# Optimization experiments

Hardware: AMD Instinct MI355X
Metric: run time of the kernel (lower is better)

## Reference

```python
import jax, jax.numpy as jnp
import numpy as np

N_HEAD = 16

def setup_inputs() -> dict:
    key = jax.random.key(0)
    k1, k2, k3 = jax.random.split(key, 3)
    B, T, C = 2, 2048, 1024
    x = jax.random.normal(k1, (B, T, C), dtype=jnp.float32)
    W_attn = jax.random.normal(k2, (C, 3 * C), dtype=jnp.float32) * (C ** -0.5)
    b_attn = jnp.zeros((3 * C,), dtype=jnp.float32)
    W_proj = jax.random.normal(k3, (C, C), dtype=jnp.float32) * (C ** -0.5)
    b_proj = jnp.zeros((C,), dtype=jnp.float32)
    return {"x": x, "W_attn": W_attn, "b_attn": b_attn, "W_proj": W_proj, "b_proj": b_proj}

def reference(x, W_attn, b_attn, W_proj, b_proj):
    B, T, C = x.shape
    H = N_HEAD
    D = C // H  # head_dim
    scale = D ** -0.5
    qkv = x @ W_attn + b_attn                       # [B,T,3C]
    q, k, v = jnp.split(qkv, 3, axis=-1)
    # [B,T,C] -> [B,H,T,D]
    q = q.reshape(B, T, H, D).transpose(0, 2, 1, 3)
    k = k.reshape(B, T, H, D).transpose(0, 2, 1, 3)
    v = v.reshape(B, T, H, D).transpose(0, 2, 1, 3)
    att = jnp.einsum('bhqd,bhkd->bhqk', q, k) * scale
    causal = jnp.tril(jnp.ones((T, T), dtype=bool))
    att = jnp.where(causal, att, jnp.float32(-jnp.inf))
    att = jax.nn.softmax(att, axis=-1)
    y = jnp.einsum('bhqk,bhkd->bhqd', att, v)       # [B,H,T,D]
    y = y.transpose(0, 2, 1, 3).reshape(B, T, C)
    return y @ W_proj + b_proj
```

## Files before the change

### kernel.cpp

```cpp
#include <hip/hip_runtime.h>

typedef __bf16 bf16;
typedef __bf16 bf16x4 __attribute__((ext_vector_type(4)));
typedef __bf16 bf16x8 __attribute__((ext_vector_type(8)));
typedef short s16x4 __attribute__((ext_vector_type(4)));
typedef float f32x4 __attribute__((ext_vector_type(4)));
typedef unsigned int u32x4 __attribute__((ext_vector_type(4)));

#define NB 2
#define NT 2048
#define NC 1024
#define NH 16
#define ND 64

#if __has_builtin(__builtin_amdgcn_exp2f)
#define EXP2F(x) __builtin_amdgcn_exp2f(x)
#else
#define EXP2F(x) __expf(0.69314718055994531f * (x))
#endif

#if __has_builtin(__builtin_amdgcn_rcpf)
#define RCPF(x) __builtin_amdgcn_rcpf(x)
#else
#define RCPF(x) (1.0f / (x))
#endif

__device__ __forceinline__ void async16(const void* g, void* l) {
  __builtin_amdgcn_global_load_lds(
      (const __attribute__((address_space(1))) void*)g,
      (__attribute__((address_space(3))) void*)l, 16, 0, 0);
}

__device__ __forceinline__ bf16x8 ld8(const bf16* p) {
  return *reinterpret_cast<const bf16x8*>(p);
}
__device__ __forceinline__ bf16x4 ld4(const bf16* p) {
  return *reinterpret_cast<const bf16x4*>(p);
}

__device__ __forceinline__ f32x4 mfma16(bf16x4 a, bf16x4 b, f32x4 c) {
  s16x4 ai = __builtin_bit_cast(s16x4, a);
  s16x4 bi = __builtin_bit_cast(s16x4, b);
#if __has_builtin(__builtin_amdgcn_mfma_f32_16x16x16bf16_1k)
  return __builtin_amdgcn_mfma_f32_16x16x16bf16_1k(ai, bi, c, 0, 0, 0);
#else
  f32x4 d;
  asm("v_mfma_f32_16x16x16_bf16 %0, %1, %2, %3"
      : "=v"(d) : "v"(ai), "v"(bi), "v"(c));
  return d;
#endif
}

__global__ __launch_bounds__(256) void prep(
    const float* __restrict__ x, bf16* __restrict__ xb,
    const float* __restrict__ Wa, bf16* __restrict__ Da,
    const float* __restrict__ Wp, bf16* __restrict__ Dp) {
  int bx = blockIdx.x;
  if (bx < 2048) {
    int i = (bx * 256 + threadIdx.x) * 8;
    const float4* s = (const float4*)(x + i);
    float4 a = s[0], b = s[1];
    bf16x8 o;
    o[0] = (bf16)a.x; o[1] = (bf16)a.y; o[2] = (bf16)a.z; o[3] = (bf16)a.w;
    o[4] = (bf16)b.x; o[5] = (bf16)b.y; o[6] = (bf16)b.z; o[7] = (bf16)b.w;
    *(bf16x8*)(xb + i) = o;
    return;
  }
  __shared__ float tile[32][33];
  int idx = bx - 2048;
  const float* src;
  bf16* dst;
  int Cc, cb, rb;
  if (idx < 96 * 32) { src = Wa; dst = Da; Cc = 3072; cb = idx % 96; rb = idx / 96; }
  else { idx -= 96 * 32; src = Wp; dst = Dp; Cc = 1024; cb = idx % 32; rb = idx / 32; }
  int tx = threadIdx.x & 31, ty = threadIdx.x >> 5;
  int r0 = rb * 32, c0 = cb * 32;
#pragma unroll
  for (int i = 0; i < 4; ++i)
    tile[ty + i * 8][tx] = src[(size_t)(r0 + ty + i * 8) * Cc + c0 + tx];
  __syncthreads();
#pragma unroll
  for (int i = 0; i < 4; ++i)
    dst[(size_t)(c0 + ty + i * 8) * 1024 + r0 + tx] = (bf16)tile[tx][ty + i * 8];
}

__global__ __launch_bounds__(256, 3) void gemm_qkv(
    const bf16* __restrict__ A,
    const bf16* __restrict__ Bt,
    const float* __restrict__ bias,
    bf16* __restrict__ Qo, bf16* __restrict__ Ko, bf16* __restrict__ Vto) {
  const int K = 1024;
  __shared__ bf16 As[128 * 32];
  __shared__ bf16 Bs[128 * 32];
  const int tid = threadIdx.x;
  const int lane = tid & 63, wv = tid >> 6;
  const int quad = lane >> 4, ln = lane & 15;
  const int m0 = blockIdx.x * 128, n0 = blockIdx.y * 128;
  const int wr = (wv >> 1) * 64, wc = (wv & 1) * 64;
  const int rA = tid >> 2, cA = (tid & 3) * 8;
  f32x4 acc[4][4] = {};

  for (int kt = 0; kt < K / 32; ++kt) {
    const int k0 = kt * 32;
#pragma unroll
    for (int inst = 0; inst < 2; ++inst) {
      async16(A + (size_t)(m0 + inst * 64 + rA) * K + k0 + cA,
              &As[inst * 2048 + wv * 512]);
      async16(Bt + (size_t)(n0 + inst * 64 + rA) * K + k0 + cA,
              &Bs[inst * 2048 + wv * 512]);
    }
    __syncthreads();
    bf16x8 aF[4], bF[4];
#pragma unroll
    for (int i = 0; i < 4; ++i) {
      aF[i] = ld8(&As[(wr + i * 16 + ln) * 32 + quad * 8]);
      bF[i] = ld8(&Bs[(wc + i * 16 + ln) * 32 + quad * 8]);
    }
#pragma unroll
    for (int rb = 0; rb < 4; ++rb)
#pragma unroll
      for (int cb = 0; cb < 4; ++cb)
        acc[rb][cb] = __builtin_amdgcn_mfma_f32_16x16x32_bf16(
            aF[rb], bF[cb], acc[rb][cb], 0, 0, 0);
    __syncthreads();
  }
#pragma unroll
  for (int rb = 0; rb < 4; ++rb) {
#pragma unroll
    for (int cb = 0; cb < 4; ++cb) {
      int gn = n0 + wc + cb * 16 + ln;
      int part = gn >> 10, c = gn & 1023;
      int h = c >> 6, dd = c & 63;
      float bs = bias[gn];
      int gm0 = m0 + wr + rb * 16 + quad * 4;
      int b = gm0 >> 11, t0 = gm0 & 2047;
      if (part == 2) {
        bf16x4 vv;
#pragma unroll
        for (int r = 0; r < 4; ++r) vv[r] = (bf16)(acc[rb][cb][r] + bs);
        *(bf16x4*)(Vto + ((size_t)(b * NH + h) * ND + dd) * NT + t0) = vv;
      } else {
        bf16* dst = part == 0 ? Qo : Ko;
        float sc = part == 0 ? 0.18033688f : 1.0f;
#pragma unroll
        for (int r = 0; r < 4; ++r)
          dst[((size_t)(b * NH + h) * NT + t0 + r) * ND + dd] =
              (bf16)((acc[rb][cb][r] + bs) * sc);
      }
    }
  }
}

__global__ __launch_bounds__(256, 3) void flash_attn_kernel(
    const bf16* __restrict__ Qg, const bf16* __restrict__ Kg,
    const bf16* __restrict__ Vtg, bf16* __restrict__ Yg) {
  __shared__ __align__(16) char smem[2][16384];
  const int tid = threadIdx.x;
  const int lane = tid & 63, wv = tid >> 6;
  const int quad = lane >> 4, ln = lane & 15;
  const int bid = blockIdx.x;
  const int qt = 15 - (bid >> 5);
  const int bh = bid & 31;
  const int bb = bh >> 4, hh = bh & 15;
  const int q0w = qt * 128 + wv * 32;
  const bf16* Qp = Qg + ((size_t)bh * NT + q0w) * ND;
  const bf16* Kbase = Kg + (size_t)bh * NT * ND;
  const bf16* Vtbase = Vtg + (size_t)bh * ND * NT;

  const int sub = lane >> 3, sch = lane & 7;
  const int swz = ln & 7;

  bf16x8 qf[2][2];
#pragma unroll
  for (int qb = 0; qb < 2; ++qb)
#pragma unroll
    for (int ks = 0; ks < 2; ++ks)
      qf[qb][ks] = ld8(Qp + (size_t)(qb * 16 + ln) * ND + ks * 32 + quad * 8);

  f32x4 oacc[2][4] = {};
  float li[2] = {0.f, 0.f};

  const int ktiles = 2 * qt + 2;
  const int cw = 2 * qt + 1 + (wv >> 1);

#define STAGE(KT, P)                                                           \
  {                                                                            \
    const int k0s = (KT) * 64;                                                 \
    char* Kl = smem[P];                                                        \
    char* Vl = smem[P] + 8192;                                                 \
    int r0s = wv * 16 + sub;                                                   \
    int gch = sch ^ sub;                                                       \
    async16(Kbase + (size_t)(k0s + r0s) * ND + gch * 8, Kl + wv * 16 * 128);   \
    async16(Kbase + (size_t)(k0s + r0s + 8) * ND + gch * 8,                    \
            Kl + wv * 16 * 128 + 1024);                                        \
    async16(Vtbase + (size_t)r0s * NT + k0s + gch * 8, Vl + wv * 16 * 128);    \
    async16(Vtbase + (size_t)(r0s + 8) * NT + k0s + gch * 8,                   \
            Vl + wv * 16 * 128 + 1024);                                        \
  }

  STAGE(0, 0);
  for (int kt = 0; kt < ktiles; ++kt) {
    const int p = kt & 1;
    __syncthreads();
    if (kt + 1 < ktiles) STAGE(kt + 1, p ^ 1);
    if (kt < cw) {
      const char* Kl = smem[p];
      const char* Vl = smem[p] + 8192;
      const int k0 = kt * 64;
      f32x4 sacc[2][4] = {};
#pragma unroll
      for (int ks = 0; ks < 2; ++ks) {
        bf16x8 kfr[4];
#pragma unroll
        for (int cb = 0; cb < 4; ++cb)
          kfr[cb] = *(const bf16x8*)(Kl + (cb * 16 + ln) * 128 +
                                     (((ks * 4 + quad) ^ swz) * 16));
#pragma unroll
        for (int qb = 0; qb < 2; ++qb)
#pragma unroll
          for (int cb = 0; cb < 4; ++cb)
            sacc[qb][cb] = __builtin_amdgcn_mfma_f32_16x16x32_bf16(
                kfr[cb], qf[qb][ks], sacc[qb][cb], 0, 0, 0);
      }
      if (k0 + 63 > q0w) {
#pragma unroll
        for (int qb = 0; qb < 2; ++qb) {
          int qr = q0w + qb * 16 + ln;
#pragma unroll
          for (int cb = 0; cb < 4; ++cb)
#pragma unroll
            for (int r = 0; r < 4; ++r) {
              int kc = k0 + cb * 16 + quad * 4 + r;
              if (kc > qr) sacc[qb][cb][r] = -1e30f;
            }
        }
      }
      bf16x4 pf[2][4];
#pragma unroll
      for (int qb = 0; qb < 2; ++qb) {
        float rs = 0.f;
#pragma unroll
        for (int cb = 0; cb < 4; ++cb) {
          bf16x4 pv;
#pragma unroll
          for (int r = 0; r < 4; ++r) {
            float pexp = EXP2F(sacc[qb][cb][r]);
            rs += pexp;
            pv[r] = (bf16)pexp;
          }
          pf[qb][cb] = pv;
        }
        li[qb] += rs;
      }
#pragma unroll
      for (int cb = 0; cb < 4; ++cb) {
        bf16x4 vfr[4];
#pragma unroll
        for (int db = 0; db < 4; ++db)
          vfr[db] = *(const bf16x4*)(Vl + (db * 16 + ln) * 128 +
                                     (((cb * 2 + (quad >> 1)) ^ swz) * 16) +
                                     (quad & 1) * 8);
#pragma unroll
        for (int qb = 0; qb < 2; ++qb)
#pragma unroll
          for (int db = 0; db < 4; ++db)
            oacc[qb][db] = mfma16(vfr[db], pf[qb][cb], oacc[qb][db]);
      }
    }
  }
#undef STAGE

#pragma unroll
  for (int qb = 0; qb < 2; ++qb) {
    float l = li[qb];
    l += __shfl_xor(l, 16);
    l += __shfl_xor(l, 32);
    float inv = RCPF(l);
    int row = q0w + qb * 16 + ln;
#pragma unroll
    for (int db = 0; db < 4; ++db) {
      bf16x4 ov;
#pragma unroll
      for (int r = 0; r < 4; ++r) ov[r] = (bf16)(oacc[qb][db][r] * inv);
      *(bf16x4*)(Yg + ((size_t)(bb * NT + row)) * NC + hh * 64 + db * 16 +
                 quad * 4) = ov;
    }
  }
}

__global__ __launch_bounds__(256, 2) void gemm_proj(
    const bf16* __restrict__ A,
    const bf16* __restrict__ Bt,
    const float* __restrict__ bias,
    float* __restrict__ out) {
  const int K = 1024;
  __shared__ bf16 As[128 * 32];
  __shared__ bf16 Bs[64 * 32];
  const int tid = threadIdx.x;
  const int lane = tid & 63, wv = tid >> 6;
  const int quad = lane >> 4, ln = lane & 15;
  const int m0 = blockIdx.x * 128, n0 = blockIdx.y * 64;
  const int wr = wv * 32;
  const int rA = tid >> 2, cA = (tid & 3) * 8;
  f32x4 acc[2][4] = {};

  for (int kt = 0; kt < K / 32; ++kt) {
    const int k0 = kt * 32;
#pragma unroll
    for (int inst = 0; inst < 2; ++inst)
      async16(A + (size_t)(m0 + inst * 64 + rA) * K + k0 + cA,
              &As[inst * 2048 + wv * 512]);
    async16(Bt + (size_t)(n0 + rA) * K + k0 + cA, &Bs[wv * 512]);
    __syncthreads();
    bf16x8 aF[2], bF[4];
#pragma unroll
    for (int i = 0; i < 2; ++i)
      aF[i] = ld8(&As[(wr + i * 16 + ln) * 32 + quad * 8]);
#pragma unroll
    for (int i = 0; i < 4; ++i)
      bF[i] = ld8(&Bs[(i * 16 + ln) * 32 + quad * 8]);
#pragma unroll
    for (int rb = 0; rb < 2; ++rb)
#pragma unroll
      for (int cb = 0; cb < 4; ++cb)
        acc[rb][cb] = __builtin_amdgcn_mfma_f32_16x16x32_bf16(
            aF[rb], bF[cb], acc[rb][cb], 0, 0, 0);
    __syncthreads();
  }
#pragma unroll
  for (int rb = 0; rb < 2; ++rb) {
#pragma unroll
    for (int cb = 0; cb < 4; ++cb) {
      int gn = n0 + cb * 16 + ln;
      float bs = bias[gn];
#pragma unroll
      for (int r = 0; r < 4; ++r) {
        int gm = m0 + wr + rb * 16 + quad * 4 + r;
        out[(size_t)gm * 1024 + gn] = acc[rb][cb][r] + bs;
      }
    }
  }
}

extern "C" void kernel_launch(void* const* d_in, const int* in_sizes, int n_in,
                              void* d_out, int out_size, void* d_ws, size_t ws_size,
                              hipStream_t stream) {
  const float* x      = (const float*)d_in[0];
  const float* W_attn = (const float*)d_in[1];
  const float* b_attn = (const float*)d_in[2];
  const float* W_proj = (const float*)d_in[3];
  const float* b_proj = (const float*)d_in[4];
  float* out = (float*)d_out;

  bf16* ws  = (bf16*)d_ws;
  bf16* xb  = ws;
  bf16* Wab = xb + (size_t)4096 * 1024;
  bf16* Wpb = Wab + (size_t)3072 * 1024;
  bf16* Qb  = Wpb + (size_t)1024 * 1024;
  bf16* Kb  = Qb + (size_t)32 * 2048 * 64;
  bf16* Vtb = Kb + (size_t)32 * 2048 * 64;
  bf16* Yb  = xb;

  prep<<<2048 + 96 * 32 + 32 * 32, 256, 0, stream>>>(x, xb, W_attn, Wab,
                                                     W_proj, Wpb);
  gemm_qkv<<<dim3(32, 24), 256, 0, stream>>>(xb, Wab, b_attn, Qb, Kb, Vtb);
  flash_attn_kernel<<<512, 256, 0, stream>>>(Qb, Kb, Vtb, Yb);
  gemm_proj<<<dim3(32, 16), 256, 0, stream>>>(Yb, Wpb, b_proj, out);
}
```

Before: 167.8 us.

## Rework QKV GEMM into 256x256 double-buffered swizzled tiles with interleaved staging

The QKV projection GEMM moves from 128x128 tiles with 256 threads and single-buffered BK=32 LDS to 256x256 tiles with 512 threads and BK=64. LDS is double-buffered and XOR-swizzled to avoid bank conflicts, and the loads for the next k-tile are interleaved with four MFMA quadrants using s_setprio and partial vmcnt waits. The aim is more operand reuse per LDS load and hiding global-load latency behind MFMA work. In exchange, the grid shrinks to 192 blocks, fewer than the CU count, and the 128KB of LDS per block limits residency to one block per CU.

Result: slower. 178.1 us (+6.1%).

```diff
diff --git a/kernel.cpp b/kernel.cpp
--- a/kernel.cpp
+++ b/kernel.cpp
@@ -33,9 +33,6 @@
 
 __device__ __forceinline__ bf16x8 ld8(const bf16* p) {
   return *reinterpret_cast<const bf16x8*>(p);
-}
-__device__ __forceinline__ bf16x4 ld4(const bf16* p) {
-  return *reinterpret_cast<const bf16x4*>(p);
 }
 
 __device__ __forceinline__ f32x4 mfma16(bf16x4 a, bf16x4 b, f32x4 c) {
@@ -49,6 +46,13 @@
       : "=v"(d) : "v"(ai), "v"(bi), "v"(c));
   return d;
 #endif
+}
+
+__device__ __forceinline__ bf16x8 ldfrag(const bf16* buf, int row, int ks,
+                                         int quad) {
+  int byte = (row * 128 + ks * 64 + quad * 16) ^ ((row & 7) << 4);
+  return *reinterpret_cast<const bf16x8*>(
+      reinterpret_cast<const char*>(buf) + byte);
 }
 
 __global__ __launch_bounds__(256) void prep(
@@ -84,68 +88,139 @@
     dst[(size_t)(c0 + ty + i * 8) * 1024 + r0 + tx] = (bf16)tile[tx][ty + i * 8];
 }
 
-__global__ __launch_bounds__(256, 3) void gemm_qkv(
+__global__ __launch_bounds__(512, 2) void gemm_qkv(
     const bf16* __restrict__ A,
     const bf16* __restrict__ Bt,
     const float* __restrict__ bias,
     bf16* __restrict__ Qo, bf16* __restrict__ Ko, bf16* __restrict__ Vto) {
-  const int K = 1024;
-  __shared__ bf16 As[128 * 32];
-  __shared__ bf16 Bs[128 * 32];
+  __shared__ __align__(16) bf16 As_[2][256 * 64];
+  __shared__ __align__(16) bf16 Bs_[2][256 * 64];
   const int tid = threadIdx.x;
   const int lane = tid & 63, wv = tid >> 6;
+  const int wm = wv >> 2, wn = wv & 3;
   const int quad = lane >> 4, ln = lane & 15;
-  const int m0 = blockIdx.x * 128, n0 = blockIdx.y * 128;
-  const int wr = (wv >> 1) * 64, wc = (wv & 1) * 64;
-  const int rA = tid >> 2, cA = (tid & 3) * 8;
-  f32x4 acc[4][4] = {};
-
-  for (int kt = 0; kt < K / 32; ++kt) {
-    const int k0 = kt * 32;
-#pragma unroll
-    for (int inst = 0; inst < 2; ++inst) {
-      async16(A + (size_t)(m0 + inst * 64 + rA) * K + k0 + cA,
-              &As[inst * 2048 + wv * 512]);
-      async16(Bt + (size_t)(n0 + inst * 64 + rA) * K + k0 + cA,
-              &Bs[inst * 2048 + wv * 512]);
-    }
-    __syncthreads();
-    bf16x8 aF[4], bF[4];
-#pragma unroll
-    for (int i = 0; i < 4; ++i) {
-      aF[i] = ld8(&As[(wr + i * 16 + ln) * 32 + quad * 8]);
-      bF[i] = ld8(&Bs[(wc + i * 16 + ln) * 32 + quad * 8]);
-    }
-#pragma unroll
-    for (int rb = 0; rb < 4; ++rb)
-#pragma unroll
-      for (int cb = 0; cb < 4; ++cb)
-        acc[rb][cb] = __builtin_amdgcn_mfma_f32_16x16x32_bf16(
-            aF[rb], bF[cb], acc[rb][cb], 0, 0, 0);
-    __syncthreads();
-  }
-#pragma unroll
-  for (int rb = 0; rb < 4; ++rb) {
-#pragma unroll
-    for (int cb = 0; cb < 4; ++cb) {
-      int gn = n0 + wc + cb * 16 + ln;
-      int part = gn >> 10, c = gn & 1023;
-      int h = c >> 6, dd = c & 63;
-      float bs = bias[gn];
-      int gm0 = m0 + wr + rb * 16 + quad * 4;
-      int b = gm0 >> 11, t0 = gm0 & 2047;
-      if (part == 2) {
-        bf16x4 vv;
-#pragma unroll
-        for (int r = 0; r < 4; ++r) vv[r] = (bf16)(acc[rb][cb][r] + bs);
-        *(bf16x4*)(Vto + ((size_t)(b * NH + h) * ND + dd) * NT + t0) = vv;
-      } else {
-        bf16* dst = part == 0 ? Qo : Ko;
-        float sc = part == 0 ? 0.18033688f : 1.0f;
-#pragma unroll
-        for (int r = 0; r < 4; ++r)
-          dst[((size_t)(b * NH + h) * NT + t0 + r) * ND + dd] =
-              (bf16)((acc[rb][cb][r] + bs) * sc);
+  const int m0 = blockIdx.x * 256, n0 = blockIdx.y * 256;
+
+#define STAGE_A(tt, h, p)                                                     \
+  {                                                                           \
+    int rl = lane >> 3, ch = (lane & 7) ^ rl;                                 \
+    const bf16* g = A + (size_t)(m0 + (h) * 128 + wv * 8 + rl) * 1024 +       \
+                    (tt) * 64 + ch * 8;                                       \
+    bf16* lp = &As_[p][((h) * 128 + wv * 8) * 64];                            \
+    async16(g, lp);                                                           \
+    async16(g + (size_t)64 * 1024, lp + 64 * 64);                             \
+  }
+#define STAGE_B(tt, h, p)                                                     \
+  {                                                                           \
+    int rl = lane >> 3, ch = (lane & 7) ^ rl;                                 \
+    const bf16* g = Bt + (size_t)(n0 + (h) * 128 + wv * 8 + rl) * 1024 +      \
+                    (tt) * 64 + ch * 8;                                       \
+    bf16* lp = &Bs_[p][((h) * 128 + wv * 8) * 64];                            \
+    async16(g, lp);                                                           \
+    async16(g + (size_t)64 * 1024, lp + 64 * 64);                             \
+  }
+
+  f32x4 acc[2][2][4][2] = {};
+  bf16x8 aF[4][2], bF0[2][2], bF1[2][2];
+
+#define MFMA_Q(MH, NH, BF)                                                    \
+  __builtin_amdgcn_s_setprio(1);                                              \
+  _Pragma("unroll") for (int ks = 0; ks < 2; ++ks)                            \
+      _Pragma("unroll") for (int mm = 0; mm < 4; ++mm)                        \
+          _Pragma("unroll") for (int nn = 0; nn < 2; ++nn)                    \
+              acc[MH][NH][mm][nn] = __builtin_amdgcn_mfma_f32_16x16x32_bf16(  \
+                  aF[mm][ks], BF[nn][ks], acc[MH][NH][mm][nn], 0, 0, 0);      \
+  __builtin_amdgcn_s_setprio(0);
+
+  STAGE_A(0, 0, 0);
+  STAGE_B(0, 0, 0);
+  STAGE_B(0, 1, 0);
+  STAGE_A(0, 1, 0);
+  asm volatile("s_waitcnt vmcnt(4)" ::: "memory");
+  __builtin_amdgcn_s_barrier();
+
+  for (int t = 0; t < 16; ++t) {
+    const bf16* Ap = As_[t & 1];
+    const bf16* Bp = Bs_[t & 1];
+    const int pn = (t & 1) ^ 1;
+    const bool more = (t + 1) < 16;
+
+#pragma unroll
+    for (int mm = 0; mm < 4; ++mm)
+#pragma unroll
+      for (int ks = 0; ks < 2; ++ks)
+        aF[mm][ks] = ldfrag(Ap, wm * 64 + mm * 16 + ln, ks, quad);
+#pragma unroll
+    for (int nn = 0; nn < 2; ++nn)
+#pragma unroll
+      for (int ks = 0; ks < 2; ++ks)
+        bF0[nn][ks] = ldfrag(Bp, wn * 32 + nn * 16 + ln, ks, quad);
+    if (more) STAGE_A(t + 1, 0, pn);
+    __builtin_amdgcn_s_barrier();
+    MFMA_Q(0, 0, bF0);
+    asm volatile("s_waitcnt vmcnt(4)" ::: "memory");
+    __builtin_amdgcn_s_barrier();
+
+#pragma unroll
+    for (int nn = 0; nn < 2; ++nn)
+#pragma unroll
+      for (int ks = 0; ks < 2; ++ks)
+        bF1[nn][ks] = ldfrag(Bp, 128 + wn * 32 + nn * 16 + ln, ks, quad);
+    if (more) STAGE_B(t + 1, 0, pn);
+    __builtin_amdgcn_s_barrier();
+    MFMA_Q(0, 1, bF1);
+    asm volatile("s_waitcnt vmcnt(4)" ::: "memory");
+    __builtin_amdgcn_s_barrier();
+
+#pragma unroll
+    for (int mm = 0; mm < 4; ++mm)
+#pragma unroll
+      for (int ks = 0; ks < 2; ++ks)
+        aF[mm][ks] = ldfrag(Ap, 128 + wm * 64 + mm * 16 + ln, ks, quad);
+    if (more) STAGE_B(t + 1, 1, pn);
+    __builtin_amdgcn_s_barrier();
+    MFMA_Q(1, 1, bF1);
+    __builtin_amdgcn_s_barrier();
+
+    if (more) STAGE_A(t + 1, 1, pn);
+    __builtin_amdgcn_s_barrier();
+    MFMA_Q(1, 0, bF0);
+    asm volatile("s_waitcnt vmcnt(4)" ::: "memory");
+    __builtin_amdgcn_s_barrier();
+  }
+#undef STAGE_A
+#undef STAGE_B
+#undef MFMA_Q
+
+#pragma unroll
+  for (int MH = 0; MH < 2; ++MH) {
+#pragma unroll
+    for (int NHh = 0; NHh < 2; ++NHh) {
+#pragma unroll
+      for (int mm = 0; mm < 4; ++mm) {
+#pragma unroll
+        for (int nn = 0; nn < 2; ++nn) {
+          int gn = n0 + NHh * 128 + wn * 32 + nn * 16 + ln;
+          int part = gn >> 10, c = gn & 1023;
+          int h = c >> 6, dd = c & 63;
+          float bs = bias[gn];
+          int gm0 = m0 + MH * 128 + wm * 64 + mm * 16 + quad * 4;
+          int b = gm0 >> 11, t0 = gm0 & 2047;
+          if (part == 2) {
+            bf16x4 vv;
+#pragma unroll
+            for (int r = 0; r < 4; ++r)
+              vv[r] = (bf16)(acc[MH][NHh][mm][nn][r] + bs);
+            *(bf16x4*)(Vto + ((size_t)(b * NH + h) * ND + dd) * NT + t0) = vv;
+          } else {
+            bf16* dst = part == 0 ? Qo : Ko;
+            float sc = part == 0 ? 0.18033688f : 1.0f;
+#pragma unroll
+            for (int r = 0; r < 4; ++r)
+              dst[((size_t)(b * NH + h) * NT + t0 + r) * ND + dd] =
+                  (bf16)((acc[MH][NHh][mm][nn][r] + bs) * sc);
+          }
+        }
       }
     }
   }
@@ -363,7 +438,7 @@
 
   prep<<<2048 + 96 * 32 + 32 * 32, 256, 0, stream>>>(x, xb, W_attn, Wab,
                                                      W_proj, Wpb);
-  gemm_qkv<<<dim3(32, 24), 256, 0, stream>>>(xb, Wab, b_attn, Qb, Kb, Vtb);
+  gemm_qkv<<<dim3(16, 12), 512, 0, stream>>>(xb, Wab, b_attn, Qb, Kb, Vtb);
   flash_attn_kernel<<<512, 256, 0, stream>>>(Qb, Kb, Vtb, Yb);
   gemm_proj<<<dim3(32, 16), 256, 0, stream>>>(Yb, Wpb, b_proj, out);
 }
```

## Pair low and high causal query tiles per block to balance attention work

Applied to the files above, without the earlier changes.

Each flash-attention block now handles two 16-row query slices per wave, one from a low query tile and one from the mirrored high tile, split into two halves. The goal is to give every block a similar amount of causal work and remove the load imbalance from blocks ordered by query tile. Each block still streams K/V up to the high tile, and the low slice switches off once it is past its causal limit. This adds divergent-free but branchy MFMA issue, and the low slice does no useful work for much of the loop.

After: 357.7 us. +113.2%, slower.

```diff
diff --git a/kernel.cpp b/kernel.cpp
--- a/kernel.cpp
+++ b/kernel.cpp
@@ -33,9 +33,6 @@
 
 __device__ __forceinline__ bf16x8 ld8(const bf16* p) {
   return *reinterpret_cast<const bf16x8*>(p);
-}
-__device__ __forceinline__ bf16x4 ld4(const bf16* p) {
-  return *reinterpret_cast<const bf16x4*>(p);
 }
 
 __device__ __forceinline__ f32x4 mfma16(bf16x4 a, bf16x4 b, f32x4 c) {
@@ -159,11 +156,15 @@
   const int lane = tid & 63, wv = tid >> 6;
   const int quad = lane >> 4, ln = lane & 15;
   const int bid = blockIdx.x;
-  const int qt = 15 - (bid >> 5);
   const int bh = bid & 31;
+  const int pr = (bid >> 5) & 7;
+  const int half = bid >> 8;
   const int bb = bh >> 4, hh = bh & 15;
-  const int q0w = qt * 128 + wv * 32;
-  const bf16* Qp = Qg + ((size_t)bh * NT + q0w) * ND;
+  const int qLo = pr, qHi = 15 - pr;
+  const int q0l = qLo * 128 + half * 64 + wv * 16;
+  const int q0h = qHi * 128 + half * 64 + wv * 16;
+  const bf16* QpL = Qg + ((size_t)bh * NT + q0l) * ND;
+  const bf16* QpH = Qg + ((size_t)bh * NT + q0h) * ND;
   const bf16* Kbase = Kg + (size_t)bh * NT * ND;
   const bf16* Vtbase = Vtg + (size_t)bh * ND * NT;
 
@@ -172,16 +173,17 @@
 
   bf16x8 qf[2][2];
 #pragma unroll
-  for (int qb = 0; qb < 2; ++qb)
-#pragma unroll
-    for (int ks = 0; ks < 2; ++ks)
-      qf[qb][ks] = ld8(Qp + (size_t)(qb * 16 + ln) * ND + ks * 32 + quad * 8);
+  for (int ks = 0; ks < 2; ++ks) {
+    qf[0][ks] = ld8(QpL + (size_t)ln * ND + ks * 32 + quad * 8);
+    qf[1][ks] = ld8(QpH + (size_t)ln * ND + ks * 32 + quad * 8);
+  }
 
   f32x4 oacc[2][4] = {};
   float li[2] = {0.f, 0.f};
 
-  const int ktiles = 2 * qt + 2;
-  const int cw = 2 * qt + 1 + (wv >> 1);
+  const int ktiles = 2 * qHi + 2;
+  const int cw0 = 2 * qLo + half + 1;
+  const int cw1 = 2 * qHi + half + 1;
 
 #define STAGE(KT, P)                                                           \
   {                                                                            \
@@ -203,7 +205,8 @@
     const int p = kt & 1;
     __syncthreads();
     if (kt + 1 < ktiles) STAGE(kt + 1, p ^ 1);
-    if (kt < cw) {
+    if (kt < cw1) {
+      const bool act0 = kt < cw0;
       const char* Kl = smem[p];
       const char* Vl = smem[p] + 8192;
       const int k0 = kt * 64;
@@ -216,41 +219,64 @@
           kfr[cb] = *(const bf16x8*)(Kl + (cb * 16 + ln) * 128 +
                                      (((ks * 4 + quad) ^ swz) * 16));
 #pragma unroll
-        for (int qb = 0; qb < 2; ++qb)
-#pragma unroll
-          for (int cb = 0; cb < 4; ++cb)
-            sacc[qb][cb] = __builtin_amdgcn_mfma_f32_16x16x32_bf16(
-                kfr[cb], qf[qb][ks], sacc[qb][cb], 0, 0, 0);
-      }
-      if (k0 + 63 > q0w) {
-#pragma unroll
-        for (int qb = 0; qb < 2; ++qb) {
-          int qr = q0w + qb * 16 + ln;
-#pragma unroll
-          for (int cb = 0; cb < 4; ++cb)
-#pragma unroll
-            for (int r = 0; r < 4; ++r) {
-              int kc = k0 + cb * 16 + quad * 4 + r;
-              if (kc > qr) sacc[qb][cb][r] = -1e30f;
-            }
+        for (int cb = 0; cb < 4; ++cb) {
+          sacc[1][cb] = __builtin_amdgcn_mfma_f32_16x16x32_bf16(
+              kfr[cb], qf[1][ks], sacc[1][cb], 0, 0, 0);
+          if (act0)
+            sacc[0][cb] = __builtin_amdgcn_mfma_f32_16x16x32_bf16(
+                kfr[cb], qf[0][ks], sacc[0][cb], 0, 0, 0);
         }
       }
+      if (k0 + 63 > q0h) {
+        int qr = q0h + ln;
+#pragma unroll
+        for (int cb = 0; cb < 4; ++cb)
+#pragma unroll
+          for (int r = 0; r < 4; ++r) {
+            int kc = k0 + cb * 16 + quad * 4 + r;
+            if (kc > qr) sacc[1][cb][r] = -1e30f;
+          }
+      }
+      if (act0 && k0 + 63 > q0l) {
+        int qr = q0l + ln;
+#pragma unroll
+        for (int cb = 0; cb < 4; ++cb)
+#pragma unroll
+          for (int r = 0; r < 4; ++r) {
+            int kc = k0 + cb * 16 + quad * 4 + r;
+            if (kc > qr) sacc[0][cb][r] = -1e30f;
+          }
+      }
       bf16x4 pf[2][4];
-#pragma unroll
-      for (int qb = 0; qb < 2; ++qb) {
+      {
         float rs = 0.f;
 #pragma unroll
         for (int cb = 0; cb < 4; ++cb) {
           bf16x4 pv;
 #pragma unroll
           for (int r = 0; r < 4; ++r) {
-            float pexp = EXP2F(sacc[qb][cb][r]);
+            float pexp = EXP2F(sacc[1][cb][r]);
             rs += pexp;
             pv[r] = (bf16)pexp;
           }
-          pf[qb][cb] = pv;
+          pf[1][cb] = pv;
         }
-        li[qb] += rs;
+        li[1] += rs;
+      }
+      if (act0) {
+        float rs = 0.f;
+#pragma unroll
+        for (int cb = 0; cb < 4; ++cb) {
+          bf16x4 pv;
+#pragma unroll
+          for (int r = 0; r < 4; ++r) {
+            float pexp = EXP2F(sacc[0][cb][r]);
+            rs += pexp;
+            pv[r] = (bf16)pexp;
+          }
+          pf[0][cb] = pv;
+        }
+        li[0] += rs;
       }
 #pragma unroll
       for (int cb = 0; cb < 4; ++cb) {
@@ -261,10 +287,12 @@
                                      (((cb * 2 + (quad >> 1)) ^ swz) * 16) +
                                      (quad & 1) * 8);
 #pragma unroll
-        for (int qb = 0; qb < 2; ++qb)
+        for (int db = 0; db < 4; ++db)
+          oacc[1][db] = mfma16(vfr[db], pf[1][cb], oacc[1][db]);
+        if (act0)
 #pragma unroll
           for (int db = 0; db < 4; ++db)
-            oacc[qb][db] = mfma16(vfr[db], pf[qb][cb], oacc[qb][db]);
+            oacc[0][db] = mfma16(vfr[db], pf[0][cb], oacc[0][db]);
       }
     }
   }
@@ -276,7 +304,7 @@
     l += __shfl_xor(l, 16);
     l += __shfl_xor(l, 32);
     float inv = RCPF(l);
-    int row = q0w + qb * 16 + ln;
+    int row = (qb ? q0h : q0l) + ln;
 #pragma unroll
     for (int db = 0; db < 4; ++db) {
       bf16x4 ov;
```

## Load K and V fragments directly from global memory, dropping LDS staging

Applied to the files above, without the earlier changes.

Removes the shared-memory double-buffered async staging of K and V tiles and the per-tile block barrier. Each wave now loads its K and V^T MFMA fragments straight from global memory into registers and iterates only over its own causal range. The launch-bounds occupancy hint drops from 3 to 2 to make room for the larger register footprint. This avoids barrier stalls and idle waves during the causal tail, but each of the 4 waves re-reads the same K/V data from global/L2 and loses the load/compute overlap.

Measured after the change: 261.2 us. +55.7%, slower.

```diff
diff --git a/kernel.cpp b/kernel.cpp
--- a/kernel.cpp
+++ b/kernel.cpp
@@ -151,10 +151,9 @@
   }
 }
 
-__global__ __launch_bounds__(256, 3) void flash_attn_kernel(
+__global__ __launch_bounds__(256, 2) void flash_attn_kernel(
     const bf16* __restrict__ Qg, const bf16* __restrict__ Kg,
     const bf16* __restrict__ Vtg, bf16* __restrict__ Yg) {
-  __shared__ __align__(16) char smem[2][16384];
   const int tid = threadIdx.x;
   const int lane = tid & 63, wv = tid >> 6;
   const int quad = lane >> 4, ln = lane & 15;
@@ -167,9 +166,6 @@
   const bf16* Kbase = Kg + (size_t)bh * NT * ND;
   const bf16* Vtbase = Vtg + (size_t)bh * ND * NT;
 
-  const int sub = lane >> 3, sch = lane & 7;
-  const int swz = ln & 7;
-
   bf16x8 qf[2][2];
 #pragma unroll
   for (int qb = 0; qb < 2; ++qb)
@@ -180,95 +176,73 @@
   f32x4 oacc[2][4] = {};
   float li[2] = {0.f, 0.f};
 
-  const int ktiles = 2 * qt + 2;
   const int cw = 2 * qt + 1 + (wv >> 1);
 
-#define STAGE(KT, P)                                                           \
-  {                                                                            \
-    const int k0s = (KT) * 64;                                                 \
-    char* Kl = smem[P];                                                        \
-    char* Vl = smem[P] + 8192;                                                 \
-    int r0s = wv * 16 + sub;                                                   \
-    int gch = sch ^ sub;                                                       \
-    async16(Kbase + (size_t)(k0s + r0s) * ND + gch * 8, Kl + wv * 16 * 128);   \
-    async16(Kbase + (size_t)(k0s + r0s + 8) * ND + gch * 8,                    \
-            Kl + wv * 16 * 128 + 1024);                                        \
-    async16(Vtbase + (size_t)r0s * NT + k0s + gch * 8, Vl + wv * 16 * 128);    \
-    async16(Vtbase + (size_t)(r0s + 8) * NT + k0s + gch * 8,                   \
-            Vl + wv * 16 * 128 + 1024);                                        \
-  }
-
-  STAGE(0, 0);
-  for (int kt = 0; kt < ktiles; ++kt) {
-    const int p = kt & 1;
-    __syncthreads();
-    if (kt + 1 < ktiles) STAGE(kt + 1, p ^ 1);
-    if (kt < cw) {
-      const char* Kl = smem[p];
-      const char* Vl = smem[p] + 8192;
-      const int k0 = kt * 64;
-      f32x4 sacc[2][4] = {};
-#pragma unroll
-      for (int ks = 0; ks < 2; ++ks) {
-        bf16x8 kfr[4];
+  for (int ksub = 0; ksub < cw; ++ksub) {
+    const int k0 = ksub * 64;
+    bf16x8 kfr[2][4];
+#pragma unroll
+    for (int ks = 0; ks < 2; ++ks)
+#pragma unroll
+      for (int cb = 0; cb < 4; ++cb)
+        kfr[ks][cb] =
+            ld8(Kbase + (size_t)(k0 + cb * 16 + ln) * ND + ks * 32 + quad * 8);
+    bf16x4 vfr[4][4];
+#pragma unroll
+    for (int cb = 0; cb < 4; ++cb)
+#pragma unroll
+      for (int db = 0; db < 4; ++db)
+        vfr[cb][db] =
+            ld4(Vtbase + (size_t)(db * 16 + ln) * NT + k0 + cb * 16 + quad * 4);
+
+    f32x4 sacc[2][4] = {};
+#pragma unroll
+    for (int ks = 0; ks < 2; ++ks)
+#pragma unroll
+      for (int qb = 0; qb < 2; ++qb)
 #pragma unroll
         for (int cb = 0; cb < 4; ++cb)
-          kfr[cb] = *(const bf16x8*)(Kl + (cb * 16 + ln) * 128 +
-                                     (((ks * 4 + quad) ^ swz) * 16));
-#pragma unroll
-        for (int qb = 0; qb < 2; ++qb)
-#pragma unroll
-          for (int cb = 0; cb < 4; ++cb)
-            sacc[qb][cb] = __builtin_amdgcn_mfma_f32_16x16x32_bf16(
-                kfr[cb], qf[qb][ks], sacc[qb][cb], 0, 0, 0);
+          sacc[qb][cb] = __builtin_amdgcn_mfma_f32_16x16x32_bf16(
+              kfr[ks][cb], qf[qb][ks], sacc[qb][cb], 0, 0, 0);
+
+    if (k0 + 63 > q0w) {
+#pragma unroll
+      for (int qb = 0; qb < 2; ++qb) {
+        int qr = q0w + qb * 16 + ln;
+#pragma unroll
+        for (int cb = 0; cb < 4; ++cb)
+#pragma unroll
+          for (int r = 0; r < 4; ++r) {
+            int kc = k0 + cb * 16 + quad * 4 + r;
+            if (kc > qr) sacc[qb][cb][r] = -1e30f;
+          }
       }
-      if (k0 + 63 > q0w) {
-#pragma unroll
-        for (int qb = 0; qb < 2; ++qb) {
-          int qr = q0w + qb * 16 + ln;
-#pragma unroll
-          for (int cb = 0; cb < 4; ++cb)
-#pragma unroll
-            for (int r = 0; r < 4; ++r) {
-              int kc = k0 + cb * 16 + quad * 4 + r;
-              if (kc > qr) sacc[qb][cb][r] = -1e30f;
-            }
+    }
+    bf16x4 pf[2][4];
+#pragma unroll
+    for (int qb = 0; qb < 2; ++qb) {
+      float rs = 0.f;
+#pragma unroll
+      for (int cb = 0; cb < 4; ++cb) {
+        bf16x4 pv;
+#pragma unroll
+        for (int r = 0; r < 4; ++r) {
+          float pexp = EXP2F(sacc[qb][cb][r]);
+          rs += pexp;
+          pv[r] = (bf16)pexp;
         }
+        pf[qb][cb] = pv;
       }
-      bf16x4 pf[2][4];
-#pragma unroll
-      for (int qb = 0; qb < 2; ++qb) {
-        float rs = 0.f;
-#pragma unroll
-        for (int cb = 0; cb < 4; ++cb) {
-          bf16x4 pv;
-#pragma unroll
-          for (int r = 0; r < 4; ++r) {
-            float pexp = EXP2F(sacc[qb][cb][r]);
-            rs += pexp;
-            pv[r] = (bf16)pexp;
-          }
-          pf[qb][cb] = pv;
-        }
-        li[qb] += rs;
-      }
-#pragma unroll
-      for (int cb = 0; cb < 4; ++cb) {
-        bf16x4 vfr[4];
+      li[qb] += rs;
+    }
+#pragma unroll
+    for (int cb = 0; cb < 4; ++cb)
+#pragma unroll
+      for (int qb = 0; qb < 2; ++qb)
 #pragma unroll
         for (int db = 0; db < 4; ++db)
-          vfr[db] = *(const bf16x4*)(Vl + (db * 16 + ln) * 128 +
-                                     (((cb * 2 + (quad >> 1)) ^ swz) * 16) +
-                                     (quad & 1) * 8);
-#pragma unroll
-        for (int qb = 0; qb < 2; ++qb)
-#pragma unroll
-          for (int db = 0; db < 4; ++db)
-            oacc[qb][db] = mfma16(vfr[db], pf[qb][cb], oacc[qb][db]);
-      }
-    }
-  }
-#undef STAGE
+          oacc[qb][db] = mfma16(vfr[cb][db], pf[qb][cb], oacc[qb][db]);
+  }
 
 #pragma unroll
   for (int qb = 0; qb < 2; ++qb) {
```
